# Optimization experiments

Hardware: AMD Instinct MI355X
Metric: run time of the kernel (lower is better)

Reference implementation:

```python
import jax, jax.numpy as jnp
import numpy as np
import math

D_MODEL = 512
D_FF = 2048
N_HEADS = 8
D_K = 64
EPS = 1e-5


def _layernorm(x, g, b):
    mu = jnp.mean(x, axis=-1, keepdims=True)
    var = jnp.mean(jnp.square(x - mu), axis=-1, keepdims=True)
    return (x - mu) * jax.lax.rsqrt(var + EPS) * g + b


def _pos_encoding(seq_len, d_model, dtype):
    pos = jnp.arange(seq_len, dtype=jnp.float32)[:, None]                 # [S,1]
    div = jnp.exp(jnp.arange(0, d_model, 2, dtype=jnp.float32) * (-math.log(10000.0) / d_model))
    ang = pos * div                                                        # [S,D/2]
    pe = jnp.stack([jnp.sin(ang), jnp.cos(ang)], axis=-1).reshape(seq_len, d_model)
    return pe.astype(dtype)


def setup_inputs() -> dict:
    key = jax.random.key(0)
    ks = jax.random.split(key, 16)
    B, S, D, F, H, DK = 4096, 16, D_MODEL, D_FF, N_HEADS, D_K
    s = lambda fan_in: 1.0 / np.sqrt(fan_in)
    u = lambda k, shp, sc: jax.random.uniform(k, shp, jnp.float32, -sc, sc)
    return {
        "enc_inputs": jax.random.normal(ks[0], (B, S, D), jnp.float32),
        # Linear weights stored as [in, out] (torch stores [out, in])
        "wq": u(ks[1], (D, H * DK), s(D)), "bq": u(ks[2], (H * DK,), s(D)),
        "wk": u(ks[3], (D, H * DK), s(D)), "bk": u(ks[4], (H * DK,), s(D)),
        "wv": u(ks[5], (D, H * DK), s(D)), "bv": u(ks[6], (H * DK,), s(D)),
        "wo": u(ks[7], (H * DK, D), s(H * DK)), "bo": u(ks[8], (D,), s(H * DK)),
        "ln1_g": jnp.ones((D,), jnp.float32), "ln1_b": jnp.zeros((D,), jnp.float32),
        "w1": u(ks[9], (D, F), s(D)), "b1": u(ks[10], (F,), s(D)),
        "w2": u(ks[11], (F, D), s(F)), "b2": u(ks[12], (D,), s(F)),
        "ln2_g": jnp.ones((D,), jnp.float32), "ln2_b": jnp.zeros((D,), jnp.float32),
        "conv_att_w": u(ks[13], (H,), s(H)),  # Conv2d(8,1,1,bias=False) == weighted head sum
    }


def reference(enc_inputs, wq, bq, wk, bk, wv, bv, wo, bo, ln1_g, ln1_b,
              w1, b1, w2, b2, ln2_g, ln2_b, conv_att_w):
    B, S, D = enc_inputs.shape
    H, DK = N_HEADS, D_K
    # positional encoding (dropout is identity in eval)
    x = enc_inputs + _pos_encoding(S, D, enc_inputs.dtype)[None, :, :]
    # multi-head self-attention
    q = (x @ wq + bq).reshape(B, S, H, DK).transpose(0, 2, 1, 3)  # [B,H,S,DK]
    k = (x @ wk + bk).reshape(B, S, H, DK).transpose(0, 2, 1, 3)
    v = (x @ wv + bv).reshape(B, S, H, DK).transpose(0, 2, 1, 3)
    scores = jnp.einsum('bhqd,bhkd->bhqk', q, k) / np.sqrt(DK)
    attn = jax.nn.softmax(scores, axis=-1)                         # [B,H,S,S]
    ctx = jnp.einsum('bhqk,bhkd->bhqd', attn, v)
    ctx = ctx.transpose(0, 2, 1, 3).reshape(B, S, H * DK)
    y = _layernorm(ctx @ wo + bo + x, ln1_g, ln1_b)
    # position-wise FFN (conv1d kernel=1 == linear)
    h = jax.nn.relu(y @ w1 + b1)
    out = _layernorm(h @ w2 + b2 + y, ln2_g, ln2_b)
    # conv_att: Conv2d(8->1, k=1, no bias) over heads
    attn_out = jnp.einsum('h,bhqk->bqk', conv_att_w, attn)
    return out, attn_out
```

## Files before the change

kernel.cpp:

```cpp
#include <hip/hip_runtime.h>
#include <hip/hip_bf16.h>

using bf16 = __hip_bfloat16;
typedef __attribute__((ext_vector_type(8))) short bf16x8;
typedef __attribute__((ext_vector_type(4))) float f32x4;

#define MFMA_BF16_16x16x32 __builtin_amdgcn_mfma_f32_16x16x32_bf16

__device__ __forceinline__ float bits2f(short b) {
  unsigned u = ((unsigned)(unsigned short)b) << 16;
  return __uint_as_float(u);
}
__device__ __forceinline__ short f2bits(float f) {
  bf16 h = __float2bfloat16(f);
  return *reinterpret_cast<short*>(&h);
}

__global__ void detect_kernel(const unsigned short* __restrict__ w, int* __restrict__ flag) {
  __shared__ int bad;
  if (threadIdx.x == 0) bad = 0;
  __syncthreads();
  float m = 0.f;
#pragma unroll
  for (int j = 0; j < 4; ++j)
    m = fmaxf(m, fabsf(bits2f((short)w[threadIdx.x * 4 + j])));
  if (m > 4.0f) atomicOr(&bad, 1);
  __syncthreads();
  if (threadIdx.x == 0) *flag = bad ? 1 : 0;
}

__global__ __launch_bounds__(256) void cvt_kernel(const void* __restrict__ src, bf16* __restrict__ dst,
                                                  int n, const int* __restrict__ flag) {
  int i = (blockIdx.x * 256 + threadIdx.x) * 8;
  if (i >= n) return;
  bf16x8 o;
  if (*flag) {
    const float* s = (const float*)src + i;
    f32x4 a = *reinterpret_cast<const f32x4*>(s);
    f32x4 b = *reinterpret_cast<const f32x4*>(s + 4);
#pragma unroll
    for (int j = 0; j < 4; ++j) { o[j] = f2bits(a[j]); o[4 + j] = f2bits(b[j]); }
  } else {
    o = *reinterpret_cast<const bf16x8*>((const bf16*)src + i);
  }
  *reinterpret_cast<bf16x8*>(dst + i) = o;
}

__global__ void pe_kernel(float* __restrict__ pe) {
  int s = blockIdx.x;
  int i = threadIdx.x;
  float dv = expf((float)(2 * i) * (-9.210340371976184f / 512.0f));
  float ang = (float)s * dv;
  pe[s * 512 + 2 * i]     = sinf(ang);
  pe[s * 512 + 2 * i + 1] = cosf(ang);
}

__global__ __launch_bounds__(256) void add_pe2_kernel(const void* __restrict__ enc_bf,
                                                      const void* __restrict__ enc_f32,
                                                      const float* __restrict__ pe,
                                                      bf16* __restrict__ x,
                                                      const int* __restrict__ flag) {
  size_t i = ((size_t)blockIdx.x * 256 + threadIdx.x) * 8;
  int col  = (int)(i & 511);
  int srow = (int)((i >> 9) & 15);
  float e[8];
  if (*flag) {
    const float* ef = (const float*)enc_f32 + i;
    f32x4 a = *reinterpret_cast<const f32x4*>(ef);
    f32x4 b = *reinterpret_cast<const f32x4*>(ef + 4);
#pragma unroll
    for (int j = 0; j < 4; ++j) { e[j] = a[j]; e[4 + j] = b[j]; }
  } else {
    bf16x8 ev = *reinterpret_cast<const bf16x8*>((const bf16*)enc_bf + i);
#pragma unroll
    for (int j = 0; j < 8; ++j) e[j] = bits2f(ev[j]);
  }
  const float* pp = pe + srow * 512 + col;
  f32x4 p0 = *reinterpret_cast<const f32x4*>(pp);
  f32x4 p1 = *reinterpret_cast<const f32x4*>(pp + 4);
  bf16x8 o;
#pragma unroll
  for (int j = 0; j < 4; ++j) o[j] = f2bits(e[j] + p0[j]);
#pragma unroll
  for (int j = 0; j < 4; ++j) o[4 + j] = f2bits(e[4 + j] + p1[j]);
  *reinterpret_cast<bf16x8*>(x + i) = o;
}

__global__ __launch_bounds__(256) void transpose_kernel(const unsigned short* __restrict__ src,
                                                        unsigned short* __restrict__ dst,
                                                        int R, int C) {
  __shared__ unsigned short t[32][33];
  int bx = blockIdx.x * 32;
  int by = blockIdx.y * 32;
  int lx = threadIdx.x & 31, ly = threadIdx.x >> 5;
#pragma unroll
  for (int i = 0; i < 4; ++i)
    t[ly + i * 8][lx] = src[(size_t)(by + ly + i * 8) * C + bx + lx];
  __syncthreads();
#pragma unroll
  for (int i = 0; i < 4; ++i)
    dst[(size_t)(bx + ly + i * 8) * R + by + lx] = t[lx][ly + i * 8];
}

template <int EPI>
__global__ __launch_bounds__(256, 2)
void gemm_bt_kernel(const bf16* __restrict__ A, const bf16* __restrict__ Bt,
                    const bf16* __restrict__ bias, const bf16* res,
                    bf16* C, int M, int N, int K) {
  constexpr int BK = 32;
  __shared__ __align__(16) char lds[2][2][128 * BK * 2];
  const int nbx = N >> 7;
  const int bx = blockIdx.x % nbx;
  const int by = blockIdx.x / nbx;
  const int m0 = by << 7, n0 = bx << 7;
  const int tid = threadIdx.x;
  const int lane = tid & 63, wid = tid >> 6;
  const int wm = (wid >> 1) << 6, wn = (wid & 1) << 6;
  const int lr = lane & 15, gq = lane >> 4;

  f32x4 acc[4][4] = {};

  auto stage = [&](int buf, int kt) {
#pragma unroll
    for (int c = 0; c < 2; ++c) {
      int off = c * 4096 + tid * 16;
      int row = off >> 6;
      int ch  = (off >> 4) & 3;
      const bf16* ga = A  + (size_t)(m0 + row) * K + kt * BK + ch * 8;
      const bf16* gb = Bt + (size_t)(n0 + row) * K + kt * BK + ch * 8;
      __builtin_amdgcn_global_load_lds((const __attribute__((address_space(1))) void*)ga,
          (__attribute__((address_space(3))) void*)&lds[buf][0][c * 4096 + wid * 1024], 16, 0, 0);
      __builtin_amdgcn_global_load_lds((const __attribute__((address_space(1))) void*)gb,
          (__attribute__((address_space(3))) void*)&lds[buf][1][c * 4096 + wid * 1024], 16, 0, 0);
    }
  };

  auto compute = [&](int buf) {
    const char* As = lds[buf][0];
    const char* Bs = lds[buf][1];
    bf16x8 af[4], bfr[4];
#pragma unroll
    for (int i = 0; i < 4; ++i) {
      af[i]  = *reinterpret_cast<const bf16x8*>(As + (wm + i * 16 + lr) * 64 + gq * 16);
      bfr[i] = *reinterpret_cast<const bf16x8*>(Bs + (wn + i * 16 + lr) * 64 + gq * 16);
    }
#pragma unroll
    for (int i = 0; i < 4; ++i)
#pragma unroll
      for (int j = 0; j < 4; ++j)
        acc[i][j] = MFMA_BF16_16x16x32(af[i], bfr[j], acc[i][j], 0, 0, 0);
  };

  stage(0, 0);
  __syncthreads();
  const int nk = K / BK;
  int buf = 0;
  for (int kt = 0; kt < nk; ++kt) {
    if (kt + 1 < nk) stage(buf ^ 1, kt + 1);
    compute(buf);
    __syncthreads();
    buf ^= 1;
  }

#pragma unroll
  for (int i = 0; i < 4; ++i) {
#pragma unroll
    for (int j = 0; j < 4; ++j) {
      int col = n0 + wn + j * 16 + lr;
      float bv = __bfloat162float(bias[col]);
#pragma unroll
      for (int r = 0; r < 4; ++r) {
        int row = m0 + wm + i * 16 + gq * 4 + r;
        float v = acc[i][j][r] + bv;
        if (EPI == 1) v = fmaxf(v, 0.0f);
        if (EPI == 2) v += __bfloat162float(res[(size_t)row * N + col]);
        C[(size_t)row * N + col] = __float2bfloat16(v);
      }
    }
  }
}

__global__ __launch_bounds__(256)
void attn_kernel(const bf16* __restrict__ qkv, const bf16* __restrict__ cw,
                 bf16* __restrict__ ctx, float* __restrict__ attn_out) {
  __shared__ __align__(16) unsigned short p_lds[4][16][16];
  __shared__ float att_lds[4][16][16];
  const int b = blockIdx.x;
  const int tid = threadIdx.x, lane = tid & 63, w = tid >> 6;
  const int lr = lane & 15, g = lane >> 4;
  const size_t qbase = (size_t)b * 16 * 1536;
  float attacc[4] = {0.f, 0.f, 0.f, 0.f};

  for (int hh = 0; hh < 2; ++hh) {
    const int h = w * 2 + hh;
    const bf16* qp = qkv + qbase + (size_t)lr * 1536 + h * 64 + g * 8;
    const bf16* kp = qp + 512;
    bf16x8 q0 = *reinterpret_cast<const bf16x8*>(qp);
    bf16x8 q1 = *reinterpret_cast<const bf16x8*>(qp + 32);
    bf16x8 k0 = *reinterpret_cast<const bf16x8*>(kp);
    bf16x8 k1 = *reinterpret_cast<const bf16x8*>(kp + 32);
    f32x4 s = {0.f, 0.f, 0.f, 0.f};
    s = MFMA_BF16_16x16x32(q0, k0, s, 0, 0, 0);
    s = MFMA_BF16_16x16x32(q1, k1, s, 0, 0, 0);
    float wgt = __bfloat162float(cw[h]);
    float p[4];
#pragma unroll
    for (int r = 0; r < 4; ++r) {
      float sv = s[r] * 0.125f;
      float mx = sv;
#pragma unroll
      for (int mm = 1; mm < 16; mm <<= 1) mx = fmaxf(mx, __shfl_xor(mx, mm, 16));
      float e = expf(sv - mx);
      float sm = e;
#pragma unroll
      for (int mm = 1; mm < 16; mm <<= 1) sm += __shfl_xor(sm, mm, 16);
      p[r] = e / sm;
      attacc[r] += wgt * p[r];
    }
#pragma unroll
    for (int r = 0; r < 4; ++r) p_lds[w][g * 4 + r][lr] = (unsigned short)f2bits(p[r]);
    __syncthreads();
    bf16x8 pa;
#pragma unroll
    for (int j = 0; j < 8; ++j) pa[j] = 0;
    if (g < 2) pa = *reinterpret_cast<const bf16x8*>(&p_lds[w][lr][g * 8]);
    const bf16* vb_base = qkv + qbase + 1024 + h * 64;
#pragma unroll
    for (int n = 0; n < 4; ++n) {
      bf16x8 vb;
#pragma unroll
      for (int j = 0; j < 8; ++j) vb[j] = 0;
      if (g < 2) {
#pragma unroll
        for (int j = 0; j < 8; ++j)
          vb[j] = *reinterpret_cast<const short*>(vb_base + (size_t)(g * 8 + j) * 1536 + n * 16 + lr);
      }
      f32x4 z = {0.f, 0.f, 0.f, 0.f};
      f32x4 d = MFMA_BF16_16x16x32(pa, vb, z, 0, 0, 0);
#pragma unroll
      for (int r = 0; r < 4; ++r)
        ctx[(size_t)(b * 16 + g * 4 + r) * 512 + h * 64 + n * 16 + lr] = __float2bfloat16(d[r]);
    }
    __syncthreads();
  }
#pragma unroll
  for (int r = 0; r < 4; ++r) att_lds[w][g * 4 + r][lr] = attacc[r];
  __syncthreads();
  const int q = tid >> 4, kk = tid & 15;
  float ssum = att_lds[0][q][kk] + att_lds[1][q][kk] + att_lds[2][q][kk] + att_lds[3][q][kk];
  attn_out[(size_t)b * 256 + q * 16 + kk] = ssum;
}

template <int F32OUT>
__global__ __launch_bounds__(256, 4)
void ln_kernel(const bf16* in, const bf16* __restrict__ gw,
               const bf16* __restrict__ bw, void* out) {
  const int row = blockIdx.x * 4 + (threadIdx.x >> 6);
  const int lane = threadIdx.x & 63;
  const bf16* rp = in + (size_t)row * 512 + lane * 8;
  bf16x8 xv = *reinterpret_cast<const bf16x8*>(rp);
  float xf[8];
#pragma unroll
  for (int j = 0; j < 8; ++j) xf[j] = bits2f(xv[j]);
  float s = 0.f;
#pragma unroll
  for (int j = 0; j < 8; ++j) s += xf[j];
#pragma unroll
  for (int o = 32; o >= 1; o >>= 1) s += __shfl_xor(s, o, 64);
  float mu = s * (1.0f / 512.0f);
  float v = 0.f;
#pragma unroll
  for (int j = 0; j < 8; ++j) { float d = xf[j] - mu; v += d * d; }
#pragma unroll
  for (int o = 32; o >= 1; o >>= 1) v += __shfl_xor(v, o, 64);
  float rs = rsqrtf(v * (1.0f / 512.0f) + 1e-5f);
  bf16x8 gv = *reinterpret_cast<const bf16x8*>(gw + lane * 8);
  bf16x8 bv = *reinterpret_cast<const bf16x8*>(bw + lane * 8);
  if (F32OUT) {
    float* op = (float*)out + (size_t)row * 512 + lane * 8;
    f32x4 o0, o1;
#pragma unroll
    for (int j = 0; j < 4; ++j) {
      o0[j] = (xf[j] - mu) * rs * bits2f(gv[j]) + bits2f(bv[j]);
      o1[j] = (xf[4 + j] - mu) * rs * bits2f(gv[4 + j]) + bits2f(bv[4 + j]);
    }
    *reinterpret_cast<f32x4*>(op) = o0;
    *reinterpret_cast<f32x4*>(op + 4) = o1;
  } else {
    bf16x8 o8;
#pragma unroll
    for (int j = 0; j < 8; ++j)
      o8[j] = f2bits((xf[j] - mu) * rs * bits2f(gv[j]) + bits2f(bv[j]));
    *reinterpret_cast<bf16x8*>((bf16*)out + (size_t)row * 512 + lane * 8) = o8;
  }
}

extern "C" void kernel_launch(void* const* d_in, const int* in_sizes, int n_in,
                              void* d_out, int out_size, void* d_ws, size_t ws_size,
                              hipStream_t stream) {
  const void* enc  = d_in[0];
  const void* wq   = d_in[1];
  const void* bq   = d_in[2];
  const void* wk   = d_in[3];
  const void* bk   = d_in[4];
  const void* wv   = d_in[5];
  const void* bvv  = d_in[6];
  const void* wo   = d_in[7];
  const void* bo   = d_in[8];
  const void* ln1g = d_in[9];
  const void* ln1b = d_in[10];
  const void* w1   = d_in[11];
  const void* b1   = d_in[12];
  const void* w2   = d_in[13];
  const void* b2   = d_in[14];
  const void* ln2g = d_in[15];
  const void* ln2b = d_in[16];
  const void* cw   = d_in[17];

  float* outp     = (float*)d_out;
  float* attn_out = outp + (size_t)33554432;

  char* wsp = (char*)d_ws;
  size_t off = 0;
  auto alloc = [&](size_t bytes) {
    void* p = wsp + off;
    off = (off + bytes + 255) & ~(size_t)255;
    return p;
  };
  int*  flag  = (int*)alloc(4);
  float* pe   = (float*)alloc((size_t)16 * 512 * 4);
  bf16* wqkvT = (bf16*)alloc((size_t)1536 * 512 * 2);
  bf16* woT   = (bf16*)alloc((size_t)512 * 512 * 2);
  bf16* w1T   = (bf16*)alloc((size_t)2048 * 512 * 2);
  bf16* w2T   = (bf16*)alloc((size_t)512 * 2048 * 2);
  bf16* stageW= (bf16*)alloc((size_t)1048576 * 2);
  bf16* bqkv  = (bf16*)alloc((size_t)1536 * 2);
  bf16* bo_c  = (bf16*)alloc((size_t)512 * 2);
  bf16* b1_c  = (bf16*)alloc((size_t)2048 * 2);
  bf16* b2_c  = (bf16*)alloc((size_t)512 * 2);
  bf16* l1g_c = (bf16*)alloc((size_t)512 * 2);
  bf16* l1b_c = (bf16*)alloc((size_t)512 * 2);
  bf16* l2g_c = (bf16*)alloc((size_t)512 * 2);
  bf16* l2b_c = (bf16*)alloc((size_t)512 * 2);
  bf16* cw_c  = (bf16*)alloc((size_t)8 * 2);
  size_t fixed_bytes = off;

  int CH = 1024;
  {
    const int cands[6] = {65536, 32768, 16384, 8192, 4096, 2048};
    for (int ci = 0; ci < 6; ++ci) {
      size_t need = fixed_bytes + (size_t)cands[ci] * 6144 + (1u << 20);
      if (need <= ws_size) { CH = cands[ci]; break; }
    }
  }
  bf16* x_c   = (bf16*)alloc((size_t)CH * 512 * 2);
  bf16* ctx_c = (bf16*)alloc((size_t)CH * 512 * 2);
  bf16* share = (bf16*)alloc((size_t)CH * 2048 * 2);
  bf16* qkv = share;
  bf16* h   = share;
  bf16* y_c = ctx_c;

  auto cvt = [&](const void* src, bf16* dst, int n) {
    cvt_kernel<<<(n + 2047) / 2048, 256, 0, stream>>>(src, dst, n, flag);
  };

  detect_kernel<<<1, 256, 0, stream>>>((const unsigned short*)wq, flag);
  pe_kernel<<<16, 256, 0, stream>>>(pe);
  cvt(wq, stageW, 262144);
  transpose_kernel<<<dim3(16, 16), 256, 0, stream>>>((const unsigned short*)stageW, (unsigned short*)wqkvT, 512, 512);
  cvt(wk, stageW, 262144);
  transpose_kernel<<<dim3(16, 16), 256, 0, stream>>>((const unsigned short*)stageW, (unsigned short*)(wqkvT + 512 * 512), 512, 512);
  cvt(wv, stageW, 262144);
  transpose_kernel<<<dim3(16, 16), 256, 0, stream>>>((const unsigned short*)stageW, (unsigned short*)(wqkvT + 1024 * 512), 512, 512);
  cvt(wo, stageW, 262144);
  transpose_kernel<<<dim3(16, 16), 256, 0, stream>>>((const unsigned short*)stageW, (unsigned short*)woT, 512, 512);
  cvt(w1, stageW, 1048576);
  transpose_kernel<<<dim3(64, 16), 256, 0, stream>>>((const unsigned short*)stageW, (unsigned short*)w1T, 512, 2048);
  cvt(w2, stageW, 1048576);
  transpose_kernel<<<dim3(16, 64), 256, 0, stream>>>((const unsigned short*)stageW, (unsigned short*)w2T, 2048, 512);
  cvt(bq, bqkv, 512);
  cvt(bk, bqkv + 512, 512);
  cvt(bvv, bqkv + 1024, 512);
  cvt(bo, bo_c, 512);
  cvt(b1, b1_c, 2048);
  cvt(b2, b2_c, 512);
  cvt(ln1g, l1g_c, 512);
  cvt(ln1b, l1b_c, 512);
  cvt(ln2g, l2g_c, 512);
  cvt(ln2b, l2b_c, 512);
  cvt(cw, cw_c, 8);

  for (int r0 = 0; r0 < 65536; r0 += CH) {
    float* out_c = outp + (size_t)r0 * 512;
    float* ao_c  = attn_out + (size_t)(r0 / 16) * 256;
    add_pe2_kernel<<<CH / 4, 256, 0, stream>>>(
        (const void*)((const bf16*)enc + (size_t)r0 * 512),
        (const void*)((const float*)enc + (size_t)r0 * 512), pe, x_c, flag);
    gemm_bt_kernel<0><<<(CH / 128) * 12, 256, 0, stream>>>(x_c, wqkvT, bqkv, nullptr, qkv, CH, 1536, 512);
    attn_kernel<<<CH / 16, 256, 0, stream>>>(qkv, cw_c, ctx_c, ao_c);
    gemm_bt_kernel<2><<<(CH / 128) * 4, 256, 0, stream>>>(ctx_c, woT, bo_c, x_c, x_c, CH, 512, 512);
    ln_kernel<0><<<CH / 4, 256, 0, stream>>>(x_c, l1g_c, l1b_c, y_c);
    gemm_bt_kernel<1><<<(CH / 128) * 16, 256, 0, stream>>>(y_c, w1T, b1_c, nullptr, h, CH, 2048, 512);
    gemm_bt_kernel<2><<<(CH / 128) * 4, 256, 0, stream>>>(h, w2T, b2_c, y_c, y_c, CH, 512, 2048);
    ln_kernel<1><<<CH / 4, 256, 0, stream>>>(y_c, l2g_c, l2b_c, out_c);
  }
}
```

Measured before the change: 901.9 us.

## Fuse weight convert with transpose, batch small converts, swizzle GEMM blocks, stage QKV in LDS

Weight conversion is folded into the transpose kernel, so the staging buffer and six convert launches go away. The eleven small bias and norm-parameter conversions become a single batched launch. GEMM workgroup IDs are remapped with an XCD-aware swizzle to improve L2 locality. The attention kernel first copies its batch's full QKV tile into LDS with vector loads, replacing strided global gathers for V. The cost is about 49KB of LDS per attention block, which may reduce occupancy.

```diff
diff --git a/kernel.cpp b/kernel.cpp
--- a/kernel.cpp
+++ b/kernel.cpp
@@ -16,6 +16,11 @@
   return *reinterpret_cast<short*>(&h);
 }
 
+__device__ __forceinline__ int xcd_swz(int bid, int nwg) {
+  int q = nwg >> 3;
+  return (bid & 7) * q + (bid >> 3);
+}
+
 __global__ void detect_kernel(const unsigned short* __restrict__ w, int* __restrict__ flag) {
   __shared__ int bad;
   if (threadIdx.x == 0) bad = 0;
@@ -27,23 +32,6 @@
   if (m > 4.0f) atomicOr(&bad, 1);
   __syncthreads();
   if (threadIdx.x == 0) *flag = bad ? 1 : 0;
-}
-
-__global__ __launch_bounds__(256) void cvt_kernel(const void* __restrict__ src, bf16* __restrict__ dst,
-                                                  int n, const int* __restrict__ flag) {
-  int i = (blockIdx.x * 256 + threadIdx.x) * 8;
-  if (i >= n) return;
-  bf16x8 o;
-  if (*flag) {
-    const float* s = (const float*)src + i;
-    f32x4 a = *reinterpret_cast<const f32x4*>(s);
-    f32x4 b = *reinterpret_cast<const f32x4*>(s + 4);
-#pragma unroll
-    for (int j = 0; j < 4; ++j) { o[j] = f2bits(a[j]); o[4 + j] = f2bits(b[j]); }
-  } else {
-    o = *reinterpret_cast<const bf16x8*>((const bf16*)src + i);
-  }
-  *reinterpret_cast<bf16x8*>(dst + i) = o;
 }
 
 __global__ void pe_kernel(float* __restrict__ pe) {
@@ -86,20 +74,39 @@
   *reinterpret_cast<bf16x8*>(x + i) = o;
 }
 
-__global__ __launch_bounds__(256) void transpose_kernel(const unsigned short* __restrict__ src,
-                                                        unsigned short* __restrict__ dst,
-                                                        int R, int C) {
+__global__ __launch_bounds__(256) void transpose_cvt_kernel(const void* __restrict__ src,
+                                                            unsigned short* __restrict__ dst,
+                                                            int R, int C, const int* __restrict__ flag) {
   __shared__ unsigned short t[32][33];
   int bx = blockIdx.x * 32;
   int by = blockIdx.y * 32;
   int lx = threadIdx.x & 31, ly = threadIdx.x >> 5;
-#pragma unroll
-  for (int i = 0; i < 4; ++i)
-    t[ly + i * 8][lx] = src[(size_t)(by + ly + i * 8) * C + bx + lx];
+  if (*flag) {
+    const float* s = (const float*)src;
+#pragma unroll
+    for (int i = 0; i < 4; ++i)
+      t[ly + i * 8][lx] = (unsigned short)f2bits(s[(size_t)(by + ly + i * 8) * C + bx + lx]);
+  } else {
+    const unsigned short* s = (const unsigned short*)src;
+#pragma unroll
+    for (int i = 0; i < 4; ++i)
+      t[ly + i * 8][lx] = s[(size_t)(by + ly + i * 8) * C + bx + lx];
+  }
   __syncthreads();
 #pragma unroll
   for (int i = 0; i < 4; ++i)
     dst[(size_t)(bx + ly + i * 8) * R + by + lx] = t[lx][ly + i * 8];
+}
+
+struct SmallSeg { const void* src; bf16* dst; int n; };
+struct SmallCvtArgs { SmallSeg seg[11]; };
+__global__ __launch_bounds__(256) void small_cvt_kernel(SmallCvtArgs a, const int* __restrict__ flag) {
+  SmallSeg s = a.seg[blockIdx.x];
+  int f = *flag;
+  for (int i = threadIdx.x; i < s.n; i += 256) {
+    float v = f ? ((const float*)s.src)[i] : bits2f(((const short*)s.src)[i]);
+    s.dst[i] = __float2bfloat16(v);
+  }
 }
 
 template <int EPI>
@@ -110,8 +117,9 @@
   constexpr int BK = 32;
   __shared__ __align__(16) char lds[2][2][128 * BK * 2];
   const int nbx = N >> 7;
-  const int bx = blockIdx.x % nbx;
-  const int by = blockIdx.x / nbx;
+  const int wg = xcd_swz(blockIdx.x, gridDim.x);
+  const int bx = wg % nbx;
+  const int by = wg / nbx;
   const int m0 = by << 7, n0 = bx << 7;
   const int tid = threadIdx.x;
   const int lane = tid & 63, wid = tid >> 6;
@@ -183,18 +191,25 @@
 __global__ __launch_bounds__(256)
 void attn_kernel(const bf16* __restrict__ qkv, const bf16* __restrict__ cw,
                  bf16* __restrict__ ctx, float* __restrict__ attn_out) {
+  __shared__ __align__(16) unsigned short qkv_lds[16][1544];
   __shared__ __align__(16) unsigned short p_lds[4][16][16];
   __shared__ float att_lds[4][16][16];
   const int b = blockIdx.x;
   const int tid = threadIdx.x, lane = tid & 63, w = tid >> 6;
   const int lr = lane & 15, g = lane >> 4;
-  const size_t qbase = (size_t)b * 16 * 1536;
+  const bf16* src = qkv + (size_t)b * 16 * 1536;
+  for (int t = tid; t < 16 * 192; t += 256) {
+    int row = t / 192, ch = t - row * 192;
+    *reinterpret_cast<bf16x8*>(&qkv_lds[row][ch * 8]) =
+        *reinterpret_cast<const bf16x8*>(src + (size_t)row * 1536 + ch * 8);
+  }
+  __syncthreads();
   float attacc[4] = {0.f, 0.f, 0.f, 0.f};
 
   for (int hh = 0; hh < 2; ++hh) {
     const int h = w * 2 + hh;
-    const bf16* qp = qkv + qbase + (size_t)lr * 1536 + h * 64 + g * 8;
-    const bf16* kp = qp + 512;
+    const unsigned short* qp = &qkv_lds[lr][h * 64 + g * 8];
+    const unsigned short* kp = qp + 512;
     bf16x8 q0 = *reinterpret_cast<const bf16x8*>(qp);
     bf16x8 q1 = *reinterpret_cast<const bf16x8*>(qp + 32);
     bf16x8 k0 = *reinterpret_cast<const bf16x8*>(kp);
@@ -224,7 +239,6 @@
 #pragma unroll
     for (int j = 0; j < 8; ++j) pa[j] = 0;
     if (g < 2) pa = *reinterpret_cast<const bf16x8*>(&p_lds[w][lr][g * 8]);
-    const bf16* vb_base = qkv + qbase + 1024 + h * 64;
 #pragma unroll
     for (int n = 0; n < 4; ++n) {
       bf16x8 vb;
@@ -233,7 +247,7 @@
       if (g < 2) {
 #pragma unroll
         for (int j = 0; j < 8; ++j)
-          vb[j] = *reinterpret_cast<const short*>(vb_base + (size_t)(g * 8 + j) * 1536 + n * 16 + lr);
+          vb[j] = (short)qkv_lds[g * 8 + j][1024 + h * 64 + n * 16 + lr];
       }
       f32x4 z = {0.f, 0.f, 0.f, 0.f};
       f32x4 d = MFMA_BF16_16x16x32(pa, vb, z, 0, 0, 0);
@@ -333,7 +347,6 @@
   bf16* woT   = (bf16*)alloc((size_t)512 * 512 * 2);
   bf16* w1T   = (bf16*)alloc((size_t)2048 * 512 * 2);
   bf16* w2T   = (bf16*)alloc((size_t)512 * 2048 * 2);
-  bf16* stageW= (bf16*)alloc((size_t)1048576 * 2);
   bf16* bqkv  = (bf16*)alloc((size_t)1536 * 2);
   bf16* bo_c  = (bf16*)alloc((size_t)512 * 2);
   bf16* b1_c  = (bf16*)alloc((size_t)2048 * 2);
@@ -360,35 +373,29 @@
   bf16* h   = share;
   bf16* y_c = ctx_c;
 
-  auto cvt = [&](const void* src, bf16* dst, int n) {
-    cvt_kernel<<<(n + 2047) / 2048, 256, 0, stream>>>(src, dst, n, flag);
-  };
-
   detect_kernel<<<1, 256, 0, stream>>>((const unsigned short*)wq, flag);
   pe_kernel<<<16, 256, 0, stream>>>(pe);
-  cvt(wq, stageW, 262144);
-  transpose_kernel<<<dim3(16, 16), 256, 0, stream>>>((const unsigned short*)stageW, (unsigned short*)wqkvT, 512, 512);
-  cvt(wk, stageW, 262144);
-  transpose_kernel<<<dim3(16, 16), 256, 0, stream>>>((const unsigned short*)stageW, (unsigned short*)(wqkvT + 512 * 512), 512, 512);
-  cvt(wv, stageW, 262144);
-  transpose_kernel<<<dim3(16, 16), 256, 0, stream>>>((const unsigned short*)stageW, (unsigned short*)(wqkvT + 1024 * 512), 512, 512);
-  cvt(wo, stageW, 262144);
-  transpose_kernel<<<dim3(16, 16), 256, 0, stream>>>((const unsigned short*)stageW, (unsigned short*)woT, 512, 512);
-  cvt(w1, stageW, 1048576);
-  transpose_kernel<<<dim3(64, 16), 256, 0, stream>>>((const unsigned short*)stageW, (unsigned short*)w1T, 512, 2048);
-  cvt(w2, stageW, 1048576);
-  transpose_kernel<<<dim3(16, 64), 256, 0, stream>>>((const unsigned short*)stageW, (unsigned short*)w2T, 2048, 512);
-  cvt(bq, bqkv, 512);
-  cvt(bk, bqkv + 512, 512);
-  cvt(bvv, bqkv + 1024, 512);
-  cvt(bo, bo_c, 512);
-  cvt(b1, b1_c, 2048);
-  cvt(b2, b2_c, 512);
-  cvt(ln1g, l1g_c, 512);
-  cvt(ln1b, l1b_c, 512);
-  cvt(ln2g, l2g_c, 512);
-  cvt(ln2b, l2b_c, 512);
-  cvt(cw, cw_c, 8);
+  transpose_cvt_kernel<<<dim3(16, 16), 256, 0, stream>>>(wq, (unsigned short*)wqkvT, 512, 512, flag);
+  transpose_cvt_kernel<<<dim3(16, 16), 256, 0, stream>>>(wk, (unsigned short*)(wqkvT + 512 * 512), 512, 512, flag);
+  transpose_cvt_kernel<<<dim3(16, 16), 256, 0, stream>>>(wv, (unsigned short*)(wqkvT + 1024 * 512), 512, 512, flag);
+  transpose_cvt_kernel<<<dim3(16, 16), 256, 0, stream>>>(wo, (unsigned short*)woT, 512, 512, flag);
+  transpose_cvt_kernel<<<dim3(64, 16), 256, 0, stream>>>(w1, (unsigned short*)w1T, 512, 2048, flag);
+  transpose_cvt_kernel<<<dim3(16, 64), 256, 0, stream>>>(w2, (unsigned short*)w2T, 2048, 512, flag);
+  {
+    SmallCvtArgs a;
+    a.seg[0]  = {bq,   bqkv,        512};
+    a.seg[1]  = {bk,   bqkv + 512,  512};
+    a.seg[2]  = {bvv,  bqkv + 1024, 512};
+    a.seg[3]  = {bo,   bo_c,        512};
+    a.seg[4]  = {b1,   b1_c,       2048};
+    a.seg[5]  = {b2,   b2_c,        512};
+    a.seg[6]  = {ln1g, l1g_c,       512};
+    a.seg[7]  = {ln1b, l1b_c,       512};
+    a.seg[8]  = {ln2g, l2g_c,       512};
+    a.seg[9]  = {ln2b, l2b_c,       512};
+    a.seg[10] = {cw,   cw_c,          8};
+    small_cvt_kernel<<<11, 256, 0, stream>>>(a, flag);
+  }
 
   for (int r0 = 0; r0 < 65536; r0 += CH) {
     float* out_c = outp + (size_t)r0 * 512;
```

Measured after the change: 863.0 us. -4.3%, faster.
